# Optimization experiments

Measured on AMD Instinct MI355X. Metric: run time of the kernel, lower is better.

The kernel has to match this reference:

```python
import jax, jax.numpy as jnp
from jax import lax
import numpy as np

NH = 4                      # num_heads in CrossScaleCom
KS = [3, 5, 7, 9]           # per-head depthwise kernel sizes
WS = 2                      # window_size in LocalFeatureGuided
GGM_K = 7                   # guide-token generator kernel size


def _dwconv(x, w, stride, pad):
    # depthwise conv: w has shape (C, 1, k, k), feature_group_count = C
    return lax.conv_general_dilated(
        x, w, (stride, stride), [(pad, pad), (pad, pad)],
        feature_group_count=x.shape[1],
        dimension_numbers=("NCHW", "OIHW", "NCHW"))


def _forward(x, dw_w0, dw_b0, dw_w1, dw_b1, dw_w2, dw_b2, dw_w3, dw_b3,
             csc_w, csc_b, bn_gamma, bn_beta, bn_mean, bn_var,
             ggm_w, ggm_b, qkv_w, qkv_b, proj_w, proj_b):
    B, C, H, W = x.shape
    cph = C // NH
    # ---- CrossScaleCom: per-head multi-scale depthwise convs ----
    xh = x.reshape(B, NH, cph, H, W)
    dws = [(dw_w0, dw_b0), (dw_w1, dw_b1), (dw_w2, dw_b2), (dw_w3, dw_b3)]
    heads = [_dwconv(xh[:, i], w, 1, KS[i] // 2) + b[None, :, None, None]
             for i, (w, b) in enumerate(dws)]
    y = jnp.stack(heads, 1)                      # (B, NH, cph, H, W)
    y = y.transpose(0, 2, 1, 3, 4).reshape(B, C, H, W)  # channel shuffle
    y = jnp.einsum("bchw,oc->bohw", y, csc_w) + csc_b[None, :, None, None]
    Co = y.shape[1]
    # ---- LocalFeatureGuided ----
    # ggm: BatchNorm (eval) -> GELU (exact) -> depthwise conv k=7 stride=WS
    inv = bn_gamma / jnp.sqrt(bn_var + 1e-5)
    g = (y - bn_mean[None, :, None, None]) * inv[None, :, None, None] \
        + bn_beta[None, :, None, None]
    g = jax.nn.gelu(g, approximate=False)
    g = _dwconv(g, ggm_w, WS, GGM_K // 2) + ggm_b[None, :, None, None]  # (B,Co,Ho,Wo)
    Ho, Wo = H // WS, W // WS
    L = Ho * Wo
    # unfold(kernel=WS, stride=WS) -> (B, Co, WS*WS, L), torch unfold ordering
    xu = y.reshape(B, Co, Ho, WS, Wo, WS).transpose(0, 1, 3, 5, 2, 4)
    xu = xu.reshape(B, Co, WS * WS, L)
    tokens = jnp.concatenate([g.reshape(B, Co, 1, L), xu], axis=2)  # (B,Co,5,L)
    # 1x1 conv over channel dim == einsum
    qkv = jnp.einsum("bcpl,oc->bopl", tokens, qkv_w) + qkv_b[None, :, None, None]
    q, k, v = jnp.split(qkv, 3, axis=1)          # each (B, Co, 5, L)
    # tiny 5x5 attention per (batch, channel), contracting over windows L
    attn = jnp.einsum("bcpl,bcql->bcpq", q, k) / (Co ** 0.5)
    attn = jax.nn.softmax(attn, axis=-1)
    out = jnp.einsum("bcpq,bcql->bcpl", attn, v)  # (B, Co, 5, L)
    out = out[:, :, 0, :].reshape(B, Co, Ho, Wo)  # guide-token output
    out = jnp.einsum("bchw,oc->bohw", out, proj_w) + proj_b[None, :, None, None]
    return out


def setup_inputs() -> dict:
    key = jax.random.key(0)
    ks = jax.random.split(key, 16)
    B, Cin, Cout, H, W = 8, 64, 128, 224, 224
    cph = Cin // NH
    s = 0.05
    d = {"x": jax.random.normal(ks[0], (B, Cin, H, W), jnp.float32)}
    for i, kk in enumerate(KS):
        d[f"dw_w{i}"] = jax.random.normal(ks[1 + i], (cph, 1, kk, kk), jnp.float32) * s
        d[f"dw_b{i}"] = jnp.zeros((cph,), jnp.float32)
    d["csc_w"] = jax.random.normal(ks[5], (Cout, Cin), jnp.float32) * s
    d["csc_b"] = jnp.zeros((Cout,), jnp.float32)
    d["bn_gamma"] = jnp.ones((Cout,), jnp.float32)
    d["bn_beta"] = jnp.zeros((Cout,), jnp.float32)
    d["bn_mean"] = jnp.zeros((Cout,), jnp.float32)
    d["bn_var"] = jnp.ones((Cout,), jnp.float32)
    d["ggm_w"] = jax.random.normal(ks[6], (Cout, 1, GGM_K, GGM_K), jnp.float32) * s
    d["ggm_b"] = jnp.zeros((Cout,), jnp.float32)
    d["qkv_w"] = jax.random.normal(ks[7], (3 * Cout, Cout), jnp.float32) * s
    d["qkv_b"] = jnp.zeros((3 * Cout,), jnp.float32)
    d["proj_w"] = jax.random.normal(ks[8], (Cout, Cout), jnp.float32) * s
    d["proj_b"] = jnp.zeros((Cout,), jnp.float32)
    return d


def reference(x, dw_w0, dw_b0, dw_w1, dw_b1, dw_w2, dw_b2, dw_w3, dw_b3,
              csc_w, csc_b, bn_gamma, bn_beta, bn_mean, bn_var,
              ggm_w, ggm_b, qkv_w, qkv_b, proj_w, proj_b):
    return _forward(x, dw_w0, dw_b0, dw_w1, dw_b1, dw_w2, dw_b2, dw_w3, dw_b3,
                    csc_w, csc_b, bn_gamma, bn_beta, bn_mean, bn_var,
                    ggm_w, ggm_b, qkv_w, qkv_b, proj_w, proj_b)
```

## Files before the change

### kernel.cpp

```cpp
#include <hip/hip_runtime.h>

#define BB 8
#define CIN 64
#define CO 128
#define Hdim 224
#define Wdim 224
#define HWt (224*224)
#define HO 112
#define WO 112
#define Lt (112*112)

typedef unsigned short u16;
typedef short bf16x8 __attribute__((ext_vector_type(8)));
typedef float f32x4  __attribute__((ext_vector_type(4)));
#define MFMA16(a,b,c) __builtin_amdgcn_mfma_f32_16x16x32_bf16((a),(b),(c),0,0,0)

__device__ inline u16 f2bf(float f) {
    union { float f; unsigned u; } v; v.f = f;
    unsigned r = (v.u + 0x7fffu + ((v.u >> 16) & 1u)) >> 16;
    return (u16)r;
}
__device__ inline float bf2f(u16 h) {
    union { unsigned u; float f; } v; v.u = ((unsigned)h) << 16; return v.f;
}
__device__ inline float uasf(unsigned u) {
    union { unsigned u; float f; } v; v.u = u; return v.f;
}
__device__ inline float sum8bf(uint4 v) {
    return bf2f(v.x & 0xffff) + bf2f(v.x >> 16) + bf2f(v.y & 0xffff) + bf2f(v.y >> 16)
         + bf2f(v.z & 0xffff) + bf2f(v.z >> 16) + bf2f(v.w & 0xffff) + bf2f(v.w >> 16);
}

__device__ inline float gelu_fast(float x) {
    float z  = x * 0.7071067811865476f;
    float az = fabsf(z);
    float t  = __builtin_amdgcn_rcpf(fmaf(0.3275911f, az, 1.0f));
    float p  = fmaf(fmaf(fmaf(fmaf(1.061405429f, t, -1.453152027f), t,
                    1.421413741f), t, -0.284496736f), t, 0.254829592f);
    float e  = __expf(-z * z);
    float er = copysignf(1.0f - p * t * e, z);
    return 0.5f * x * (1.0f + er);
}

__global__ void zero_kernel(float* __restrict__ p, int n4) {
    int i = blockIdx.x * 256 + threadIdx.x;
    if (i < n4) ((float4*)p)[i] = make_float4(0.f, 0.f, 0.f, 0.f);
}

template<int HEAD>
__global__ __launch_bounds__(256) void dw_conv(
    const float* __restrict__ x, const float* __restrict__ w,
    const float* __restrict__ bias, u16* __restrict__ dwb)
{
    constexpr int K   = 3 + 2*HEAD;
    constexpr int PAD = HEAD + 1;
    constexpr int R   = 32 + 2*PAD;
    const int tile = blockIdx.x;
    const int c    = blockIdx.y;
    const int b    = blockIdx.z;
    const int th = (tile/7)*32, tw = (tile%7)*32;
    __shared__ float patch[R*40];
    const int tid = threadIdx.x;
    const float* xin = x + (size_t)(b*CIN + HEAD*16 + c)*HWt;
    for (int idx = tid; idx < R*40; idx += 256) {
        int r = idx / 40, cc = idx - r*40;
        int gy = th - PAD + r, gx = tw - 4 + cc;
        float v = 0.f;
        if (gy >= 0 && gy < Hdim && gx >= 0 && gx < Wdim) v = xin[gy*Wdim + gx];
        patch[idx] = v;
    }
    float wreg[K*K];
    const float* wp = w + c*K*K;
    #pragma unroll
    for (int i = 0; i < K*K; i++) wreg[i] = wp[i];
    const float bv = bias[c];
    __syncthreads();

    const int ty = tid >> 3, x0 = (tid & 7) * 4;
    float acc[4] = {bv, bv, bv, bv};
    #pragma unroll
    for (int ky = 0; ky < K; ky++) {
        float rr[12];
        *(float4*)&rr[0] = *(const float4*)&patch[(ty+ky)*40 + x0];
        *(float4*)&rr[4] = *(const float4*)&patch[(ty+ky)*40 + x0 + 4];
        *(float4*)&rr[8] = *(const float4*)&patch[(ty+ky)*40 + x0 + 8];
        #pragma unroll
        for (int kx = 0; kx < K; kx++) {
            const float wv = wreg[ky*K + kx];
            #pragma unroll
            for (int j = 0; j < 4; j++)
                acc[j] = fmaf(rr[j + kx + 4 - PAD], wv, acc[j]);
        }
    }
    const int s = c*4 + HEAD;
    u16 o4[4] = {f2bf(acc[0]), f2bf(acc[1]), f2bf(acc[2]), f2bf(acc[3])};
    *(uint2*)&dwb[(size_t)(b*CIN + s)*HWt + (th+ty)*Wdim + tw + x0] = *(uint2*)o4;
}

__global__ __launch_bounds__(256) void csc_mfma(
    const float* __restrict__ W, const float* __restrict__ bias,
    const u16* __restrict__ dwb, u16* __restrict__ y4)
{
    const int b  = blockIdx.z;
    const int p0 = blockIdx.x * 128;
    __shared__ u16 Abuf[128*72];
    __shared__ u16 Tbuf[32*132];
    const int tid = threadIdx.x;
    const int wv = tid >> 6, ln = tid & 63;
    const int mh = (wv >> 1)*64, nh = (wv & 1)*64;
    const int lm = ln & 15, kq = ln >> 4;
    for (int t = tid; t < 1024; t += 256) {
        int r = t >> 3, kk = (t & 7)*8;
        const float* src = &W[r*64 + kk];
        float4 f0 = *(const float4*)src, f1 = *(const float4*)(src+4);
        u16 tmp[8] = {f2bf(f0.x),f2bf(f0.y),f2bf(f0.z),f2bf(f0.w),
                      f2bf(f1.x),f2bf(f1.y),f2bf(f1.z),f2bf(f1.w)};
        *(uint4*)&Abuf[r*72 + kk] = *(uint4*)tmp;
    }
    const u16* Db = dwb + (size_t)b*CIN*HWt;
    f32x4 acc[4][4];
    #pragma unroll
    for (int i=0;i<4;i++)
        #pragma unroll
        for (int j=0;j<4;j++) acc[i][j] = (f32x4){0.f,0.f,0.f,0.f};

    for (int kc = 0; kc < 64; kc += 32) {
        __syncthreads();
        for (int t = tid; t < 512; t += 256) {
            int k = t >> 4, n0 = (t & 15)*8;
            *(uint4*)&Tbuf[k*132 + n0] = *(const uint4*)&Db[(size_t)(kc+k)*HWt + p0 + n0];
        }
        __syncthreads();
        bf16x8 af[4], bfr[4];
        #pragma unroll
        for (int tm=0;tm<4;tm++)
            af[tm] = *(bf16x8*)&Abuf[(mh + tm*16 + lm)*72 + kc + kq*8];
        #pragma unroll
        for (int tn=0;tn<4;tn++) {
            int n = nh + tn*16 + lm;
            #pragma unroll
            for (int j=0;j<8;j++) bfr[tn][j] = (short)Tbuf[(kq*8+j)*132 + n];
        }
        #pragma unroll
        for (int tm=0;tm<4;tm++)
            #pragma unroll
            for (int tn=0;tn<4;tn++)
                acc[tm][tn] = MFMA16(af[tm], bfr[tn], acc[tm][tn]);
    }
    #pragma unroll
    for (int tm=0;tm<4;tm++) {
        #pragma unroll
        for (int r=0;r<4;r++) {
            int o = mh + tm*16 + kq*4 + r;
            float bb = bias[o];
            #pragma unroll
            for (int tn=0;tn<4;tn++) {
                int p = p0 + nh + tn*16 + lm;
                int gy = p / 224, gx = p - gy*224;
                int w = (gy&1)*2 + (gx&1);
                y4[((size_t)(b*CO + o)*4 + w)*Lt + (gy>>1)*WO + (gx>>1)]
                    = f2bf(acc[tm][tn][r] + bb);
            }
        }
    }
}

__global__ __launch_bounds__(256) void ggm_kernel(const u16* __restrict__ y4,
    const float* __restrict__ gamma, const float* __restrict__ beta,
    const float* __restrict__ mean, const float* __restrict__ var,
    const float* __restrict__ gw, const float* __restrict__ gb,
    u16* __restrict__ gbf)
{
    const int ho0 = blockIdx.x * 16;
    const int c   = blockIdx.y;
    const int b   = blockIdx.z;
    __shared__ float patch[37*240];
    const int tid = threadIdx.x;

    const float inv = gamma[c] * rsqrtf(var[c] + 1e-5f);
    const float bsh = fmaf(-mean[c], inv, beta[c]);
    const u16* ybc = y4 + (size_t)(b*CO + c)*4*Lt;

    float wk[49];
    const float* wp = gw + c*49;
    #pragma unroll
    for (int i = 0; i < 49; i++) wk[i] = wp[i];
    const float bv = gb[c];

    for (int idx = tid; idx < 37*60; idx += 256) {
        int r = idx / 60, j = idx - r*60;
        int gy = 2*ho0 - 3 + r;
        float4 v = make_float4(0.f, 0.f, 0.f, 0.f);
        if (gy >= 0 && gy < Hdim && j >= 2 && j <= 57) {
            const u16* pe = ybc + (size_t)((gy&1)*2)*Lt + (gy>>1)*WO + (2*j - 4);
            unsigned e = *(const unsigned*)pe;
            unsigned o = *(const unsigned*)(pe + Lt);
            v.x = gelu_fast(fmaf(uasf(e << 16),         inv, bsh));
            v.y = gelu_fast(fmaf(uasf(o << 16),         inv, bsh));
            v.z = gelu_fast(fmaf(uasf(e & 0xffff0000u), inv, bsh));
            v.w = gelu_fast(fmaf(uasf(o & 0xffff0000u), inv, bsh));
        }
        *(float4*)&patch[idx*4] = v;
    }
    __syncthreads();

    if (tid < 224) {
        const int n = tid % 56;
        const int g = tid / 56;
        float acc[4][2];
        #pragma unroll
        for (int i = 0; i < 4; i++) { acc[i][0] = bv; acc[i][1] = bv; }
        #pragma unroll
        for (int rr = 0; rr < 13; rr++) {
            const float* row = &patch[(8*g + rr)*240 + 4*n + 4];
            float f[12];
            *(float4*)&f[0] = *(const float4*)&row[0];
            *(float4*)&f[4] = *(const float4*)&row[4];
            *(float4*)&f[8] = *(const float4*)&row[8];
            #pragma unroll
            for (int i = 0; i < 4; i++) {
                const int ky = rr - 2*i;
                if (ky >= 0 && ky <= 6) {
                    #pragma unroll
                    for (int kx = 0; kx < 7; kx++) {
                        const float wv = wk[ky*7 + kx];
                        acc[i][0] = fmaf(f[kx + 1], wv, acc[i][0]);
                        acc[i][1] = fmaf(f[kx + 3], wv, acc[i][1]);
                    }
                }
            }
        }
        u16* gout = gbf + (size_t)(b*CO + c)*Lt;
        #pragma unroll
        for (int i = 0; i < 4; i++) {
            u16 o2[2] = {f2bf(acc[i][0]), f2bf(acc[i][1])};
            *(unsigned*)&gout[(ho0 + 4*g + i)*WO + 2*n] = *(unsigned*)o2;
        }
    }
}

__global__ __launch_bounds__(256) void G_mfma(
    const u16* __restrict__ gbf, const u16* __restrict__ y4,
    float* __restrict__ G)
{
    const int b = blockIdx.z, p = blockIdx.y, split = blockIdx.x;
    const u16* Ab = gbf + (size_t)b*CO*Lt;
    const u16* Bb; int brs;
    if (p == 0) { Bb = Ab; brs = Lt; }
    else        { Bb = y4 + ((size_t)b*CO*4 + (p-1))*Lt; brs = 4*Lt; }
    __shared__ u16 Abuf[128*40];
    __shared__ u16 Bbuf[128*40];
    const int tid = threadIdx.x;
    const int wv = tid >> 6, ln = tid & 63;
    const int mh = (wv >> 1)*64, nh = (wv & 1)*64;
    const int lm = ln & 15, kq = ln >> 4;
    f32x4 acc[4][4];
    #pragma unroll
    for (int i=0;i<4;i++)
        #pragma unroll
        for (int j=0;j<4;j++) acc[i][j] = (f32x4){0.f,0.f,0.f,0.f};

    for (int ci = split; ci < 392; ci += 32) {
        const int l0 = ci*32;
        __syncthreads();
        for (int t = tid; t < 512; t += 256) {
            int r = t >> 2, kk = (t & 3)*8;
            *(uint4*)&Abuf[r*40 + kk] = *(const uint4*)&Ab[(size_t)r*Lt  + l0 + kk];
            *(uint4*)&Bbuf[r*40 + kk] = *(const uint4*)&Bb[(size_t)r*brs + l0 + kk];
        }
        __syncthreads();
        bf16x8 af[4], bfr[4];
        #pragma unroll
        for (int tm=0;tm<4;tm++)
            af[tm]  = *(bf16x8*)&Abuf[(mh + tm*16 + lm)*40 + kq*8];
        #pragma unroll
        for (int tn=0;tn<4;tn++)
            bfr[tn] = *(bf16x8*)&Bbuf[(nh + tn*16 + lm)*40 + kq*8];
        #pragma unroll
        for (int tm=0;tm<4;tm++)
            #pragma unroll
            for (int tn=0;tn<4;tn++)
                acc[tm][tn] = MFMA16(af[tm], bfr[tn], acc[tm][tn]);
    }
    float* Go = G + ((size_t)(b*5 + p))*CO*CO;
    #pragma unroll
    for (int tm=0;tm<4;tm++)
        #pragma unroll
        for (int r=0;r<4;r++) {
            int mrow = mh + tm*16 + kq*4 + r;
            #pragma unroll
            for (int tn=0;tn<4;tn++)
                atomicAdd(&Go[mrow*CO + nh + tn*16 + lm], acc[tm][tn][r]);
        }
}

__global__ void S_kernel(const u16* __restrict__ gbf, const u16* __restrict__ y4,
                         float* __restrict__ S)
{
    const int b = blockIdx.x >> 7, c = blockIdx.x & 127;
    const u16* gr = gbf + (size_t)(b*CO+c)*Lt;
    const u16* yr = y4  + (size_t)(b*CO+c)*4*Lt;
    float vals[5] = {0.f,0.f,0.f,0.f,0.f};
    for (int i = threadIdx.x*8; i < Lt; i += 256*8)
        vals[0] += sum8bf(*(const uint4*)&gr[i]);
    #pragma unroll
    for (int w=0; w<4; w++)
        for (int i = threadIdx.x*8; i < Lt; i += 256*8)
            vals[1+w] += sum8bf(*(const uint4*)&yr[(size_t)w*Lt + i]);
    #pragma unroll
    for (int off=32; off>0; off>>=1) {
        #pragma unroll
        for (int q=0;q<5;q++) vals[q] += __shfl_down(vals[q], off);
    }
    __shared__ float red[4][5];
    const int wid = threadIdx.x>>6, lane = threadIdx.x&63;
    if (lane==0) {
        #pragma unroll
        for (int q=0;q<5;q++) red[wid][q] = vals[q];
    }
    __syncthreads();
    if (threadIdx.x==0) {
        #pragma unroll
        for (int q=0;q<5;q++)
            S[((size_t)b*5 + q)*CO + c] = red[0][q]+red[1][q]+red[2][q]+red[3][q];
    }
}

__global__ __launch_bounds__(256) void fused_logits_kernel(
    const float* __restrict__ G, const float* __restrict__ S,
    const float* __restrict__ qkv_w, const float* __restrict__ qkv_b,
    float* __restrict__ lg)
{
    const int p = blockIdx.x, b = blockIdx.y;
    __shared__ float Wl[32*132];
    __shared__ float Al[32*132];
    __shared__ float KGl[128*128];
    const int tid = threadIdx.x;
    const int og = (tid >> 4) * 8;
    const int pg = (tid & 15) * 8;
    const float* Gp = G + (size_t)(b*5 + p)*CO*CO;
    float acc[8][8];
    #pragma unroll
    for (int i=0;i<8;i++)
        #pragma unroll
        for (int j=0;j<8;j++) acc[i][j]=0.f;

    for (int kc = 0; kc < 128; kc += 32) {
        __syncthreads();
        for (int t = tid; t < 4096; t += 256) {
            int kk = t & 31, o = t >> 5;
            Wl[kk*132 + o] = Gp[(size_t)o*CO + kc + kk];
            Al[kk*132 + o] = qkv_w[(size_t)(CO + o)*CO + kc + kk];
        }
        __syncthreads();
        #pragma unroll 4
        for (int kk = 0; kk < 32; kk++) {
            float wv[8], av[8];
            *(float4*)&wv[0] = *(const float4*)&Wl[kk*132+og];
            *(float4*)&wv[4] = *(const float4*)&Wl[kk*132+og+4];
            *(float4*)&av[0] = *(const float4*)&Al[kk*132+pg];
            *(float4*)&av[4] = *(const float4*)&Al[kk*132+pg+4];
            #pragma unroll
            for (int i=0;i<8;i++)
                #pragma unroll
                for (int j=0;j<8;j++)
                    acc[i][j] = fmaf(wv[i], av[j], acc[i][j]);
        }
    }
    #pragma unroll
    for (int i=0;i<8;i++) {
        #pragma unroll
        for (int j=0;j<8;j+=4)
            *(float4*)&KGl[(og+i)*128 + pg + j] = *(float4*)&acc[i][j];
    }
    __syncthreads();
    if (tid < 128) {
        const int c = tid;
        const float qb = qkv_b[c], kb = qkv_b[CO + c];
        const float* S0 = S + (size_t)b*5*CO;
        const float* Sp = S0 + p*CO;
        const float* qwrow = qkv_w + (size_t)c*CO;
        const float* kwrow = qkv_w + (size_t)(CO + c)*CO;
        float sq = qb * 12544.f, ks = 0.f, s = 0.f;
        for (int c2 = 0; c2 < CO; c2++) {
            sq = fmaf(qwrow[c2], S0[c2], sq);
            ks = fmaf(kwrow[c2], Sp[c2], ks);
            s  = fmaf(qwrow[c2], KGl[c2*128 + c], s);
        }
        lg[(size_t)(b*5 + p)*CO + c] = s + qb*ks + kb*sq;
    }
}

__global__ void softmax5_kernel(const float* __restrict__ lg, float* __restrict__ a)
{
    const int b = blockIdx.x, c = threadIdx.x;
    float v[5];
    #pragma unroll
    for (int p=0;p<5;p++) v[p] = lg[(size_t)(b*5 + p)*CO + c];
    const float scl = 0.08838834764831845f;
    float mx = v[0];
    #pragma unroll
    for (int p=1;p<5;p++) mx = fmaxf(mx, v[p]);
    float e[5], sum = 0.f;
    #pragma unroll
    for (int p=0;p<5;p++){ e[p] = __expf((v[p]-mx)*scl); sum += e[p]; }
    const float rs = 1.f/sum;
    #pragma unroll
    for (int p=0;p<5;p++) a[((size_t)b*CO + c)*5 + p] = e[p]*rs;
}

__global__ void F_kernel(const float* __restrict__ proj_w,
    const float* __restrict__ qkv_w, const float* __restrict__ a,
    float* __restrict__ F)
{
    const int b = blockIdx.z, p = blockIdx.y;
    const int o  = blockIdx.x*2 + (threadIdx.x>>7);
    const int cp = threadIdx.x & 127;
    const float* vw = qkv_w + 2*CO*CO;
    float s = 0.f;
    for (int c=0;c<CO;c++)
        s = fmaf(proj_w[o*CO+c] * a[((size_t)b*CO+c)*5 + p], vw[c*CO+cp], s);
    F[(((size_t)(b*5+p))*CO + o)*CO + cp] = s;
}

__global__ void bias_kernel(const float* __restrict__ proj_w,
    const float* __restrict__ proj_b, const float* __restrict__ qkv_b,
    float* __restrict__ biasout)
{
    const int o = threadIdx.x;
    const float* vb = qkv_b + 2*CO;
    float s = proj_b[o];
    for (int c=0;c<CO;c++) s = fmaf(proj_w[o*CO+c], vb[c], s);
    biasout[o] = s;
}

__global__ __launch_bounds__(256) void final_mfma(
    const float* __restrict__ F, const u16* __restrict__ gbf,
    const u16* __restrict__ y4, const float* __restrict__ biasout,
    float* __restrict__ out)
{
    const int b = blockIdx.z;
    const int p0 = blockIdx.x * 128;
    __shared__ u16 Abuf[128*40];
    __shared__ u16 Tbuf[32*132];
    const int tid = threadIdx.x;
    const int wv = tid >> 6, ln = tid & 63;
    const int mh = (wv >> 1)*64, nh = (wv & 1)*64;
    const int lm = ln & 15, kq = ln >> 4;
    f32x4 acc[4][4];
    #pragma unroll
    for (int i=0;i<4;i++)
        #pragma unroll
        for (int j=0;j<4;j++) acc[i][j] = (f32x4){0.f,0.f,0.f,0.f};

    for (int ph = 0; ph < 5; ph++) {
        const float* Fp = F + (size_t)(b*5 + ph)*CO*CO;
        const u16* Bb; int brs;
        if (ph == 0) { Bb = gbf + (size_t)b*CO*Lt; brs = Lt; }
        else         { Bb = y4 + ((size_t)b*CO*4 + (ph-1))*Lt; brs = 4*Lt; }
        for (int kc = 0; kc < CO; kc += 32) {
            __syncthreads();
            for (int t = tid; t < 512; t += 256) {
                int r = t >> 2, kk = (t & 3)*8;
                const float* src = &Fp[r*CO + kc + kk];
                float4 f0 = *(const float4*)src, f1 = *(const float4*)(src+4);
                u16 tmp[8] = {f2bf(f0.x),f2bf(f0.y),f2bf(f0.z),f2bf(f0.w),
                              f2bf(f1.x),f2bf(f1.y),f2bf(f1.z),f2bf(f1.w)};
                *(uint4*)&Abuf[r*40 + kk] = *(uint4*)tmp;
            }
            for (int t = tid; t < 512; t += 256) {
                int k = t >> 4, n0 = (t & 15)*8;
                *(uint4*)&Tbuf[k*132 + n0] = *(const uint4*)&Bb[(size_t)(kc+k)*brs + p0 + n0];
            }
            __syncthreads();
            bf16x8 af[4], bfr[4];
            #pragma unroll
            for (int tm=0;tm<4;tm++)
                af[tm] = *(bf16x8*)&Abuf[(mh + tm*16 + lm)*40 + kq*8];
            #pragma unroll
            for (int tn=0;tn<4;tn++) {
                int n = nh + tn*16 + lm;
                #pragma unroll
                for (int j=0;j<8;j++) bfr[tn][j] = (short)Tbuf[(kq*8+j)*132 + n];
            }
            #pragma unroll
            for (int tm=0;tm<4;tm++)
                #pragma unroll
                for (int tn=0;tn<4;tn++)
                    acc[tm][tn] = MFMA16(af[tm], bfr[tn], acc[tm][tn]);
        }
    }
    float* Ob = out + (size_t)b*CO*Lt;
    #pragma unroll
    for (int tm=0;tm<4;tm++) {
        #pragma unroll
        for (int r=0;r<4;r++) {
            int o = mh + tm*16 + kq*4 + r;
            float bb = biasout[o];
            #pragma unroll
            for (int tn=0;tn<4;tn++)
                Ob[(size_t)o*Lt + p0 + nh + tn*16 + lm] = acc[tm][tn][r] + bb;
        }
    }
}

extern "C" void kernel_launch(void* const* d_in, const int* in_sizes, int n_in,
                              void* d_out, int out_size, void* d_ws, size_t ws_size,
                              hipStream_t stream) {
    const float* x      = (const float*)d_in[0];
    const float* dw_w0  = (const float*)d_in[1];
    const float* dw_b0  = (const float*)d_in[2];
    const float* dw_w1  = (const float*)d_in[3];
    const float* dw_b1  = (const float*)d_in[4];
    const float* dw_w2  = (const float*)d_in[5];
    const float* dw_b2  = (const float*)d_in[6];
    const float* dw_w3  = (const float*)d_in[7];
    const float* dw_b3  = (const float*)d_in[8];
    const float* csc_w  = (const float*)d_in[9];
    const float* csc_b  = (const float*)d_in[10];
    const float* bn_g   = (const float*)d_in[11];
    const float* bn_b   = (const float*)d_in[12];
    const float* bn_m   = (const float*)d_in[13];
    const float* bn_v   = (const float*)d_in[14];
    const float* ggm_w  = (const float*)d_in[15];
    const float* ggm_b  = (const float*)d_in[16];
    const float* qkv_w  = (const float*)d_in[17];
    const float* qkv_b  = (const float*)d_in[18];
    const float* proj_w = (const float*)d_in[19];
    const float* proj_b = (const float*)d_in[20];
    float* out = (float*)d_out;

    char* ws = (char*)d_ws;
    u16*   y4  = (u16*)(ws);
    u16*   dwb = (u16*)(ws + 102760448);
    u16*   gbf = (u16*)(ws + 154140672);
    float* G   = (float*)(ws + 179830784);
    float* lgb = G  + 655360;
    float* F   = lgb + 5120;
    float* S   = F  + 655360;
    float* aw  = S  + 5120;
    float* bo  = aw + 5120;

    zero_kernel<<<dim3(640), 256, 0, stream>>>(G, 655360/4);

    dw_conv<0><<<dim3(49, 16, 8), 256, 0, stream>>>(x, dw_w0, dw_b0, dwb);
    dw_conv<1><<<dim3(49, 16, 8), 256, 0, stream>>>(x, dw_w1, dw_b1, dwb);
    dw_conv<2><<<dim3(49, 16, 8), 256, 0, stream>>>(x, dw_w2, dw_b2, dwb);
    dw_conv<3><<<dim3(49, 16, 8), 256, 0, stream>>>(x, dw_w3, dw_b3, dwb);

    csc_mfma<<<dim3(392, 1, 8), 256, 0, stream>>>(csc_w, csc_b, dwb, y4);

    ggm_kernel<<<dim3(7, 128, 8), 256, 0, stream>>>(
        y4, bn_g, bn_b, bn_m, bn_v, ggm_w, ggm_b, gbf);

    G_mfma<<<dim3(32, 5, 8), 256, 0, stream>>>(gbf, y4, G);

    S_kernel<<<dim3(1024), 256, 0, stream>>>(gbf, y4, S);

    fused_logits_kernel<<<dim3(5, 8), 256, 0, stream>>>(G, S, qkv_w, qkv_b, lgb);

    softmax5_kernel<<<dim3(8), 128, 0, stream>>>(lgb, aw);

    F_kernel<<<dim3(64, 5, 8), 256, 0, stream>>>(proj_w, qkv_w, aw, F);
    bias_kernel<<<dim3(1), 128, 0, stream>>>(proj_w, proj_b, qkv_b, bo);

    final_mfma<<<dim3(98, 1, 8), 256, 0, stream>>>(F, gbf, y4, bo, out);
}
```

Before: 693.8 us.

## Replace atomic G accumulation with split-K partial buffers and a reduce kernel

The G Gram-matrix GEMM previously zeroed G and atomically added float results from 32 K-splits. It now uses 16 splits with a 64-wide K chunk per shared-memory stage (two MFMA k-steps per sync), writes each split's partial tile to a scratch buffer that reuses the dwb workspace, and sums the partials in a separate reduce kernel. This removes the zero kernel and the atomic contention and halves the barrier count per K element. In exchange it adds a partial-buffer write and read plus an extra launch, and halves the number of GEMM blocks.

```diff
diff --git a/kernel.cpp b/kernel.cpp
--- a/kernel.cpp
+++ b/kernel.cpp
@@ -40,11 +40,6 @@
     float e  = __expf(-z * z);
     float er = copysignf(1.0f - p * t * e, z);
     return 0.5f * x * (1.0f + er);
-}
-
-__global__ void zero_kernel(float* __restrict__ p, int n4) {
-    int i = blockIdx.x * 256 + threadIdx.x;
-    if (i < n4) ((float4*)p)[i] = make_float4(0.f, 0.f, 0.f, 0.f);
 }
 
 template<int HEAD>
@@ -241,15 +236,15 @@
 
 __global__ __launch_bounds__(256) void G_mfma(
     const u16* __restrict__ gbf, const u16* __restrict__ y4,
-    float* __restrict__ G)
+    float* __restrict__ Gpart)
 {
     const int b = blockIdx.z, p = blockIdx.y, split = blockIdx.x;
     const u16* Ab = gbf + (size_t)b*CO*Lt;
     const u16* Bb; int brs;
     if (p == 0) { Bb = Ab; brs = Lt; }
     else        { Bb = y4 + ((size_t)b*CO*4 + (p-1))*Lt; brs = 4*Lt; }
-    __shared__ u16 Abuf[128*40];
-    __shared__ u16 Bbuf[128*40];
+    __shared__ u16 Abuf[128*72];
+    __shared__ u16 Bbuf[128*72];
     const int tid = threadIdx.x;
     const int wv = tid >> 6, ln = tid & 63;
     const int mh = (wv >> 1)*64, nh = (wv & 1)*64;
@@ -260,29 +255,32 @@
         #pragma unroll
         for (int j=0;j<4;j++) acc[i][j] = (f32x4){0.f,0.f,0.f,0.f};
 
-    for (int ci = split; ci < 392; ci += 32) {
-        const int l0 = ci*32;
+    for (int ci = split; ci < 196; ci += 16) {
+        const int l0 = ci*64;
         __syncthreads();
-        for (int t = tid; t < 512; t += 256) {
-            int r = t >> 2, kk = (t & 3)*8;
-            *(uint4*)&Abuf[r*40 + kk] = *(const uint4*)&Ab[(size_t)r*Lt  + l0 + kk];
-            *(uint4*)&Bbuf[r*40 + kk] = *(const uint4*)&Bb[(size_t)r*brs + l0 + kk];
+        for (int t = tid; t < 1024; t += 256) {
+            int r = t >> 3, kk = (t & 7)*8;
+            *(uint4*)&Abuf[r*72 + kk] = *(const uint4*)&Ab[(size_t)r*Lt  + l0 + kk];
+            *(uint4*)&Bbuf[r*72 + kk] = *(const uint4*)&Bb[(size_t)r*brs + l0 + kk];
         }
         __syncthreads();
-        bf16x8 af[4], bfr[4];
-        #pragma unroll
-        for (int tm=0;tm<4;tm++)
-            af[tm]  = *(bf16x8*)&Abuf[(mh + tm*16 + lm)*40 + kq*8];
-        #pragma unroll
-        for (int tn=0;tn<4;tn++)
-            bfr[tn] = *(bf16x8*)&Bbuf[(nh + tn*16 + lm)*40 + kq*8];
-        #pragma unroll
-        for (int tm=0;tm<4;tm++)
+        #pragma unroll
+        for (int ks = 0; ks < 2; ks++) {
+            bf16x8 af[4], bfr[4];
+            #pragma unroll
+            for (int tm=0;tm<4;tm++)
+                af[tm]  = *(bf16x8*)&Abuf[(mh + tm*16 + lm)*72 + ks*32 + kq*8];
             #pragma unroll
             for (int tn=0;tn<4;tn++)
-                acc[tm][tn] = MFMA16(af[tm], bfr[tn], acc[tm][tn]);
-    }
-    float* Go = G + ((size_t)(b*5 + p))*CO*CO;
+                bfr[tn] = *(bf16x8*)&Bbuf[(nh + tn*16 + lm)*72 + ks*32 + kq*8];
+            #pragma unroll
+            for (int tm=0;tm<4;tm++)
+                #pragma unroll
+                for (int tn=0;tn<4;tn++)
+                    acc[tm][tn] = MFMA16(af[tm], bfr[tn], acc[tm][tn]);
+        }
+    }
+    float* Go = Gpart + ((size_t)(split*40) + b*5 + p)*CO*CO;
     #pragma unroll
     for (int tm=0;tm<4;tm++)
         #pragma unroll
@@ -290,8 +288,21 @@
             int mrow = mh + tm*16 + kq*4 + r;
             #pragma unroll
             for (int tn=0;tn<4;tn++)
-                atomicAdd(&Go[mrow*CO + nh + tn*16 + lm], acc[tm][tn][r]);
-        }
+                Go[mrow*CO + nh + tn*16 + lm] = acc[tm][tn][r];
+        }
+}
+
+__global__ void G_reduce(const float* __restrict__ Gpart, float* __restrict__ G)
+{
+    const int bp = blockIdx.x;
+    const int i4 = (blockIdx.y*256 + threadIdx.x)*4;
+    float4 s = make_float4(0.f, 0.f, 0.f, 0.f);
+    #pragma unroll
+    for (int sp = 0; sp < 16; sp++) {
+        float4 v = *(const float4*)&Gpart[((size_t)(sp*40) + bp)*CO*CO + i4];
+        s.x += v.x; s.y += v.y; s.z += v.z; s.w += v.w;
+    }
+    *(float4*)&G[(size_t)bp*CO*CO + i4] = s;
 }
 
 __global__ void S_kernel(const u16* __restrict__ gbf, const u16* __restrict__ y4,
@@ -540,8 +551,7 @@
     float* S   = F  + 655360;
     float* aw  = S  + 5120;
     float* bo  = aw + 5120;
-
-    zero_kernel<<<dim3(640), 256, 0, stream>>>(G, 655360/4);
+    float* Gpart = (float*)(ws + 102760448);
 
     dw_conv<0><<<dim3(49, 16, 8), 256, 0, stream>>>(x, dw_w0, dw_b0, dwb);
     dw_conv<1><<<dim3(49, 16, 8), 256, 0, stream>>>(x, dw_w1, dw_b1, dwb);
@@ -553,7 +563,8 @@
     ggm_kernel<<<dim3(7, 128, 8), 256, 0, stream>>>(
         y4, bn_g, bn_b, bn_m, bn_v, ggm_w, ggm_b, gbf);
 
-    G_mfma<<<dim3(32, 5, 8), 256, 0, stream>>>(gbf, y4, G);
+    G_mfma<<<dim3(16, 5, 8), 256, 0, stream>>>(gbf, y4, Gpart);
+    G_reduce<<<dim3(40, 16), 256, 0, stream>>>(Gpart, G);
 
     S_kernel<<<dim3(1024), 256, 0, stream>>>(gbf, y4, S);
 
```

Result: faster. 626.4 us (-9.7%).
